# Kernel optimization log

Measured on AMD Instinct MI355X. Metric: run time of the kernel, lower is better.

## Reference

```python
import jax, jax.numpy as jnp
import numpy as np

N = 50000          # nodes
E_RAND = 800000    # random edges
E = E_RAND + N     # + self loops -> 850000
F_IN = 256         # nembed
F_HID = 64         # nhid
H = 8              # nheads
NCLASS = 40
ALPHA = 0.2        # leakyrelu slope


def setup_inputs() -> dict:
    key = jax.random.key(0)
    ks = jax.random.split(key, 8)
    x = jax.random.normal(ks[0], (N, F_IN), dtype=jnp.float32)
    # random edges + self loops (guarantees every row-sum > 0, like adj + I)
    er = jax.random.randint(ks[1], (2, E_RAND), 0, N, dtype=jnp.int32)
    loops = jnp.tile(jnp.arange(N, dtype=jnp.int32)[None, :], (2, 1))
    edge_index = jnp.concatenate([er, loops], axis=1)  # [2, E]
    # per-head attention params (xavier-ish scale)
    W = jax.random.normal(ks[2], (H, F_IN, F_HID), dtype=jnp.float32) * (1.0 / np.sqrt(F_IN))
    a = jax.random.normal(ks[3], (H, 2 * F_HID), dtype=jnp.float32) * 0.1
    Wo = jax.random.normal(ks[4], (H * F_HID, F_HID), dtype=jnp.float32) * (1.0 / np.sqrt(H * F_HID))
    ao = jax.random.normal(ks[5], (2 * F_HID,), dtype=jnp.float32) * 0.1
    mlp_w = jax.random.normal(ks[6], (NCLASS, F_HID), dtype=jnp.float32) * 0.05
    mlp_b = jnp.zeros((NCLASS,), dtype=jnp.float32)
    return {"x": x, "edge_index": edge_index, "W": W, "a": a,
            "Wo": Wo, "ao": ao, "mlp_w": mlp_w, "mlp_b": mlp_b}


def _leaky(v):
    return jnp.where(v > 0, v, ALPHA * v)


def _spgat_layer(x, W, a, src, dst, n):
    """pyGAT SpGraphAttentionLayer (eval mode, dropout = identity).
    out[i] = sum_{e: src=i} exp(-leakyrelu(a.[h_src;h_dst])) * h[dst] / rowsum_i
    """
    h = x @ W                         # [N, D]
    D = W.shape[1]
    s_src = h @ a[:D]                 # [N]
    s_dst = h @ a[D:]                 # [N]
    # per-edge unnormalized attention (note the -exp(leaky) of original sp impl)
    e = jnp.exp(-_leaky(s_src[src] + s_dst[dst]))          # [E]
    rowsum = jax.ops.segment_sum(e, src, num_segments=n)   # [N]
    num = jax.ops.segment_sum(e[:, None] * h[dst], src, num_segments=n)  # [N, D]
    return num / rowsum[:, None]


def reference(x, edge_index, W, a, Wo, ao, mlp_w, mlp_b):
    src, dst = edge_index[0], edge_index[1]
    # multi-head attention, concat=True -> elu inside each head
    heads = [jax.nn.elu(_spgat_layer(x, W[i], a[i], src, dst, N)) for i in range(H)]
    xc = jnp.concatenate(heads, axis=1)                     # [N, H*F_HID]
    # dropout (eval) = identity
    xo = jax.nn.elu(_spgat_layer(xc, Wo, ao, src, dst, N))  # [N, F_HID]
    return xo @ mlp_w.T + mlp_b                             # [N, NCLASS]
```

## Files before the change

kernel.cpp:

```cpp
#include <hip/hip_runtime.h>

#define NN 50000
#define HH 8
#define ALPHA 0.2f
#define NPAD 50048

typedef short short8 __attribute__((ext_vector_type(8)));
typedef float f32x4 __attribute__((ext_vector_type(4)));

__device__ __forceinline__ float elu_f(float x) {
  return x > 0.f ? x : __expf(x) - 1.f;
}

__device__ __forceinline__ unsigned short f2bf(float f) {
  unsigned int u = __float_as_uint(f);
  unsigned int r = (u + 0x7fffu + ((u >> 16) & 1u)) >> 16;
  return (unsigned short)r;
}

__global__ void cvt_all_kernel(const float* __restrict__ x, unsigned short* __restrict__ xb,
                               const float* __restrict__ W, unsigned short* __restrict__ Wtc,
                               const float* __restrict__ Wo, unsigned short* __restrict__ Wot,
                               int* __restrict__ cnt, int N) {
  int tid = blockIdx.x * 256 + threadIdx.x;
  int n4x = NPAD * 64;
  if (tid < n4x) {
    int row = tid >> 6;
    ushort4 o;
    if (row < N) {
      float4 v = ((const float4*)x)[tid];
      o.x = f2bf(v.x); o.y = f2bf(v.y); o.z = f2bf(v.z); o.w = f2bf(v.w);
    } else {
      o.x = o.y = o.z = o.w = 0;
    }
    ((ushort4*)xb)[tid] = o;
    return;
  }
  int t1 = tid - n4x;
  if (t1 < 512 * 256) {
    int c = t1 >> 8, k = t1 & 255;
    int h = c >> 6, cc = c & 63;
    Wtc[t1] = f2bf(W[((size_t)h * 256 + k) * 64 + cc]);
    return;
  }
  int t2 = t1 - 512 * 256;
  if (t2 < 64 * 512) {
    int c = t2 >> 9, k = t2 & 511;
    Wot[t2] = f2bf(Wo[(size_t)k * 64 + c]);
    return;
  }
  int t3 = t2 - 64 * 512;
  if (t3 < N) cnt[t3] = 0;
}

__global__ void hist_kernel(const int* __restrict__ src, int* __restrict__ cnt, int E) {
  int e = blockIdx.x * blockDim.x + threadIdx.x;
  if (e < E) atomicAdd(&cnt[src[e]], 1);
}

__global__ __launch_bounds__(1024) void scan_fused_kernel(const int* __restrict__ cnt,
    int* __restrict__ row_ptr, int* __restrict__ nxt, int n, int E) {
  __shared__ int sh[1024];
  __shared__ int wsum[16];
  __shared__ int base_sh;
  int bid = blockIdx.x;
  int i = (bid << 10) + threadIdx.x;
  int v = (i < n) ? cnt[i] : 0;

  int lim = bid << 10;
  int s = 0;
  for (int q = threadIdx.x; q < lim; q += 1024) s += cnt[q];
#pragma unroll
  for (int off = 1; off < 64; off <<= 1) s += __shfl_xor(s, off, 64);
  if ((threadIdx.x & 63) == 0) wsum[threadIdx.x >> 6] = s;
  sh[threadIdx.x] = v;
  __syncthreads();
  if (threadIdx.x == 0) {
    int t = 0;
#pragma unroll
    for (int j = 0; j < 16; ++j) t += wsum[j];
    base_sh = t;
  }
  for (int off = 1; off < 1024; off <<= 1) {
    int t = (threadIdx.x >= off) ? sh[threadIdx.x - off] : 0;
    __syncthreads();
    sh[threadIdx.x] += t;
    __syncthreads();
  }
  if (i < n) {
    int r = base_sh + sh[threadIdx.x] - v;
    row_ptr[i] = r;
    nxt[i] = r;
  }
  if (i == 0) row_ptr[n] = E;
}

__global__ __launch_bounds__(256) void scatter_gemm1_kernel(
    const int* __restrict__ src, const int* __restrict__ dst,
    int* __restrict__ nxt, int* __restrict__ colv, int E, int eb,
    const unsigned short* __restrict__ A, const unsigned short* __restrict__ Wtc,
    const float* __restrict__ Aatt, unsigned short* __restrict__ Cout,
    float* __restrict__ ss, float* __restrict__ sd, int N) {
  __shared__ unsigned short As[128][40];
  __shared__ unsigned short Bs[128][40];

  if (blockIdx.x < (unsigned)eb) {
    int e = blockIdx.x * 256 + threadIdx.x;
    if (e < E) {
      int p = atomicAdd(&nxt[src[e]], 1);
      colv[p] = dst[e];
    }
    return;
  }

  int tile = blockIdx.x - eb;
  int m0 = (tile >> 2) * 128;
  int c0 = (tile & 3) * 128;
  int w = threadIdx.x >> 6, L = threadIdx.x & 63;
  int quad = L >> 4, l16 = L & 15;
  int wr = w >> 1, wc = w & 1;
  int y = (tile & 3) * 2 + wc;

  f32x4 acc[4][4];
#pragma unroll
  for (int mt = 0; mt < 4; ++mt)
#pragma unroll
    for (int nt = 0; nt < 4; ++nt) acc[mt][nt] = (f32x4)(0.f);

  int sr0 = threadIdx.x >> 2;
  int sk0 = (threadIdx.x & 3) << 3;

  for (int k0 = 0; k0 < 256; k0 += 32) {
    __syncthreads();
    *(uint4*)&As[sr0][sk0]      = *(const uint4*)(A + (size_t)(m0 + sr0) * 256 + k0 + sk0);
    *(uint4*)&As[sr0 + 64][sk0] = *(const uint4*)(A + (size_t)(m0 + sr0 + 64) * 256 + k0 + sk0);
    *(uint4*)&Bs[sr0][sk0]      = *(const uint4*)(Wtc + (size_t)(c0 + sr0) * 256 + k0 + sk0);
    *(uint4*)&Bs[sr0 + 64][sk0] = *(const uint4*)(Wtc + (size_t)(c0 + sr0 + 64) * 256 + k0 + sk0);
    __syncthreads();

    short8 af[4], bf[4];
#pragma unroll
    for (int mt = 0; mt < 4; ++mt)
      af[mt] = *(const short8*)&As[wr * 64 + mt * 16 + l16][quad * 8];
#pragma unroll
    for (int nt = 0; nt < 4; ++nt)
      bf[nt] = *(const short8*)&Bs[wc * 64 + nt * 16 + l16][quad * 8];
#pragma unroll
    for (int mt = 0; mt < 4; ++mt)
#pragma unroll
      for (int nt = 0; nt < 4; ++nt)
        acc[mt][nt] = __builtin_amdgcn_mfma_f32_16x16x32_bf16(af[mt], bf[nt], acc[mt][nt], 0, 0, 0);
  }

  float as[4], ad[4];
#pragma unroll
  for (int nt = 0; nt < 4; ++nt) {
    as[nt] = Aatt[y * 128 + l16 + 16 * nt];
    ad[nt] = Aatt[y * 128 + 64 + l16 + 16 * nt];
  }
#pragma unroll
  for (int mt = 0; mt < 4; ++mt) {
#pragma unroll
    for (int reg = 0; reg < 4; ++reg) {
      int row = m0 + wr * 64 + mt * 16 + quad * 4 + reg;
      float p = 0.f, q = 0.f;
#pragma unroll
      for (int nt = 0; nt < 4; ++nt) {
        p += acc[mt][nt][reg] * as[nt];
        q += acc[mt][nt][reg] * ad[nt];
      }
#pragma unroll
      for (int off = 1; off < 16; off <<= 1) {
        p += __shfl_xor(p, off, 64);
        q += __shfl_xor(q, off, 64);
      }
      if (l16 == 0 && row < N) {
        ss[(size_t)row * 8 + y] = p;
        sd[(size_t)row * 8 + y] = q;
      }
      if (row < N) {
#pragma unroll
        for (int nt = 0; nt < 4; ++nt)
          Cout[(size_t)row * 512 + y * 64 + l16 + 16 * nt] = f2bf(acc[mt][nt][reg]);
      }
    }
  }
}

__global__ __launch_bounds__(256) void mfma_gemm2_kernel(
    const unsigned short* __restrict__ A, const unsigned short* __restrict__ Bt,
    const float* __restrict__ Aatt, unsigned short* __restrict__ Cout,
    float* __restrict__ ss, float* __restrict__ sd, int N) {
  __shared__ unsigned short Bs[64][520];
  unsigned short* stage = &Bs[0][0];
  {
    for (int c = threadIdx.x; c < 4096; c += 256) {
      int n = c >> 6;
      int kq = (c & 63) << 3;
      *(uint4*)&Bs[n][kq] = *(const uint4*)(Bt + (size_t)n * 512 + kq);
    }
  }
  __syncthreads();

  int w = threadIdx.x >> 6, L = threadIdx.x & 63;
  int quad = L >> 4, l16 = L & 15;
  int m0 = blockIdx.x * 64;
  int myrow = m0 + w * 16 + l16;
  const unsigned short* Ar = A + (size_t)myrow * 512 + quad * 8;

  f32x4 acc[4];
#pragma unroll
  for (int nt = 0; nt < 4; ++nt) acc[nt] = (f32x4)(0.f);

  short8 a_cur = *(const short8*)(Ar);
  for (int k0 = 0; k0 < 512; k0 += 32) {
    short8 a_nxt;
    if (k0 + 32 < 512) a_nxt = *(const short8*)(Ar + k0 + 32);
#pragma unroll
    for (int nt = 0; nt < 4; ++nt) {
      short8 b = *(const short8*)&Bs[l16 + 16 * nt][k0 + quad * 8];
      acc[nt] = __builtin_amdgcn_mfma_f32_16x16x32_bf16(a_cur, b, acc[nt], 0, 0, 0);
    }
    a_cur = a_nxt;
  }

  float as[4], ad[4];
#pragma unroll
  for (int nt = 0; nt < 4; ++nt) {
    as[nt] = Aatt[l16 + 16 * nt];
    ad[nt] = Aatt[64 + l16 + 16 * nt];
  }
#pragma unroll
  for (int reg = 0; reg < 4; ++reg) {
    float p = 0.f, q = 0.f;
#pragma unroll
    for (int nt = 0; nt < 4; ++nt) {
      p += acc[nt][reg] * as[nt];
      q += acc[nt][reg] * ad[nt];
    }
#pragma unroll
    for (int off = 1; off < 16; off <<= 1) {
      p += __shfl_xor(p, off, 64);
      q += __shfl_xor(q, off, 64);
    }
    int row = m0 + w * 16 + quad * 4 + reg;
    if (l16 == 0 && row < N) { ss[row] = p; sd[row] = q; }
  }

  __syncthreads();
#pragma unroll
  for (int reg = 0; reg < 4; ++reg) {
    int lrow = w * 16 + quad * 4 + reg;
#pragma unroll
    for (int nt = 0; nt < 4; ++nt)
      stage[lrow * 72 + l16 + 16 * nt] = f2bf(acc[nt][reg]);
  }
  __syncthreads();
#pragma unroll
  for (int i = 0; i < 2; ++i) {
    int idx = threadIdx.x + 256 * i;
    int row = idx >> 3;
    int c8 = (idx & 7) << 3;
    if (m0 + row < N) {
      uint4 v = *(const uint4*)&stage[row * 72 + c8];
      *(uint4*)(Cout + ((size_t)(m0 + row)) * 64 + c8) = v;
    }
  }
}

__global__ __launch_bounds__(256) void agg1_kernel(const unsigned short* __restrict__ table,
    const float* __restrict__ ss, const float* __restrict__ sd,
    const int* __restrict__ row_ptr, const int* __restrict__ col,
    unsigned short* __restrict__ xc, int N) {
  int bid = blockIdx.x;
  int r8 = bid & 7;
  int p = r8 >> 2;
  int nb = ((bid >> 3) << 2) | (r8 & 3);
  int wid = threadIdx.x >> 6, L = threadIdx.x & 63;
  int n = nb * 4 + wid;
  if (n >= N) return;
  int hq = L >> 4;
  int h = p * 4 + hq;
  int el = L & 15;
  float ssn = ss[n * 8 + h];
  int k0 = row_ptr[n], deg = row_ptr[n + 1] - k0;
  float acc[4] = {0.f, 0.f, 0.f, 0.f};
  float rs = 0.f;
  const char* tb = (const char*)table + p * 512;

  for (int c0 = 0; c0 < deg; c0 += 64) {
    int j = c0 + L;
    int d_l = (j < deg) ? col[k0 + j] : 0;
    int m = min(64, deg - c0);
    for (int g = 0; g < m; g += 16) {
      int eoff = g + el;
      int de = __shfl(d_l, eoff, 64);
      float s = ssn + sd[(size_t)de * 8 + h];
      float e = __expf(-fmaxf(s, ALPHA * s));
      if (eoff >= m) e = 0.f;
      rs += e;
      int gm = min(16, m - g);
      uint2 rv[16];
#pragma unroll
      for (int t = 0; t < 16; ++t) {
        if (t < gm) {
          int dg = __builtin_amdgcn_readlane(d_l, g + t);
          rv[t] = *(const uint2*)(tb + (size_t)dg * 1024 + L * 8);
        }
      }
#pragma unroll
      for (int t = 0; t < 16; ++t) {
        if (t < gm) {
          float ew = __shfl(e, (hq << 4) + t, 64);
          acc[0] += ew * __uint_as_float(rv[t].x << 16);
          acc[1] += ew * __uint_as_float(rv[t].x & 0xffff0000u);
          acc[2] += ew * __uint_as_float(rv[t].y << 16);
          acc[3] += ew * __uint_as_float(rv[t].y & 0xffff0000u);
        }
      }
    }
  }
  rs += __shfl_xor(rs, 1, 64);
  rs += __shfl_xor(rs, 2, 64);
  rs += __shfl_xor(rs, 4, 64);
  rs += __shfl_xor(rs, 8, 64);
  float inv = 1.f / rs;
  ushort4 pk;
  pk.x = f2bf(elu_f(acc[0] * inv));
  pk.y = f2bf(elu_f(acc[1] * inv));
  pk.z = f2bf(elu_f(acc[2] * inv));
  pk.w = f2bf(elu_f(acc[3] * inv));
  *(ushort4*)(xc + (size_t)n * 512 + p * 256 + L * 4) = pk;
}

__global__ __launch_bounds__(256) void agg2_final_kernel(const unsigned short* __restrict__ table,
    const float* __restrict__ ss, const float* __restrict__ sd,
    const int* __restrict__ row_ptr, const int* __restrict__ col,
    const float* __restrict__ mlp_w, const float* __restrict__ mlp_b,
    float* __restrict__ out, int N) {
  __shared__ float wsh[40 * 65];
  __shared__ float bsh[40];
  __shared__ float osh[4][68];
  for (int i = threadIdx.x; i < 40 * 64; i += 256) wsh[(i >> 6) * 65 + (i & 63)] = mlp_w[i];
  if (threadIdx.x < 40) bsh[threadIdx.x] = mlp_b[threadIdx.x];
  __syncthreads();

  int wid = threadIdx.x >> 6, L = threadIdx.x & 63;
  int n = blockIdx.x * 4 + wid;
  bool act = (n < N);
  float o = 0.f;
  if (act) {
    float ssn = ss[n];
    int k0 = row_ptr[n], deg = row_ptr[n + 1] - k0;
    float acc = 0.f, rs = 0.f;
    const char* base = (const char*)table;
    for (int c0 = 0; c0 < deg; c0 += 64) {
      int j = c0 + L;
      int d_l = 0;
      float e_l = 0.f;
      if (j < deg) {
        d_l = col[k0 + j];
        float s = ssn + sd[d_l];
        e_l = __expf(-fmaxf(s, ALPHA * s));
      }
      rs += e_l;
      int m = min(64, deg - c0);
      int off_l = d_l << 7;
      for (int g = 0; g < m; g += 16) {
        int gm = min(16, m - g);
        unsigned hv[16];
#pragma unroll
        for (int t = 0; t < 16; ++t) {
          if (t < gm) {
            int so = __builtin_amdgcn_readlane(off_l, g + t);
            hv[t] = *(const unsigned short*)(base + so + L * 2);
          }
        }
#pragma unroll
        for (int t = 0; t < 16; ++t) {
          if (t < gm) {
            float ew = __uint_as_float(
                (unsigned)__builtin_amdgcn_readlane(__float_as_uint(e_l), g + t));
            acc += ew * __uint_as_float(hv[t] << 16);
          }
        }
      }
    }
#pragma unroll
    for (int off = 1; off < 64; off <<= 1) rs += __shfl_xor(rs, off, 64);
    o = elu_f(acc / rs);
  }
  osh[wid][L] = o;
  __syncthreads();
  if (act && L < 40) {
    const float* wr = wsh + L * 65;
    const float* orow = osh[wid];
    float acc = bsh[L];
#pragma unroll
    for (int j = 0; j < 64; ++j) acc += orow[j] * wr[j];
    out[(size_t)n * 40 + L] = acc;
  }
}

extern "C" void kernel_launch(void* const* d_in, const int* in_sizes, int n_in,
                              void* d_out, int out_size, void* d_ws, size_t ws_size,
                              hipStream_t stream) {
  (void)n_in; (void)out_size; (void)ws_size;
  const float* x  = (const float*)d_in[0];
  const int*   ei = (const int*)d_in[1];
  const float* W  = (const float*)d_in[2];
  const float* a  = (const float*)d_in[3];
  const float* Wo = (const float*)d_in[4];
  const float* ao = (const float*)d_in[5];
  const float* mw = (const float*)d_in[6];
  const float* mb = (const float*)d_in[7];
  float* out = (float*)d_out;

  const int N = NN;
  const int E = in_sizes[1] / 2;
  const int* src = ei;
  const int* dst = ei + E;

  char* ws = (char*)d_ws;
  size_t off = 0;
  auto alloc = [&](size_t bytes) {
    char* p = ws + off;
    off = (off + bytes + 255) & ~(size_t)255;
    return p;
  };
  unsigned short* xb  = (unsigned short*)alloc((size_t)NPAD * 256 * 2);
  unsigned short* Wtc = (unsigned short*)alloc((size_t)512 * 256 * 2);
  unsigned short* Wot = (unsigned short*)alloc((size_t)64 * 512 * 2);
  unsigned short* h1b = (unsigned short*)alloc((size_t)N * 512 * 2);
  float* ss1     = (float*)alloc((size_t)N * 8 * 4);
  float* sd1     = (float*)alloc((size_t)N * 8 * 4);
  unsigned short* xc = (unsigned short*)alloc((size_t)NPAD * 512 * 2);
  unsigned short* h2b = (unsigned short*)alloc((size_t)N * 64 * 2);
  float* ss2     = (float*)alloc((size_t)N * 4);
  float* sd2     = (float*)alloc((size_t)N * 4);
  int*   row_ptr = (int*)  alloc((size_t)(N + 1) * 4);
  int*   nxt     = (int*)  alloc((size_t)N * 4);
  int*   cnt     = (int*)  alloc((size_t)N * 4);
  int*   colv    = (int*)  alloc((size_t)E * 4);

  int eb = (E + 255) / 256;
  int nb1024 = (N + 1023) / 1024;
  int cvt_total = NPAD * 64 + 512 * 256 + 64 * 512 + N;
  int gtiles = (NPAD / 128) * 4;

  hipLaunchKernelGGL(cvt_all_kernel, dim3((cvt_total + 255) / 256), dim3(256), 0, stream,
                     x, xb, W, Wtc, Wo, Wot, cnt, N);

  hipLaunchKernelGGL(hist_kernel, dim3(eb), dim3(256), 0, stream, src, cnt, E);
  hipLaunchKernelGGL(scan_fused_kernel, dim3(nb1024), dim3(1024), 0, stream,
                     cnt, row_ptr, nxt, N, E);

  hipLaunchKernelGGL(scatter_gemm1_kernel, dim3(eb + gtiles), dim3(256), 0, stream,
                     src, dst, nxt, colv, E, eb,
                     xb, Wtc, a, h1b, ss1, sd1, N);

  hipLaunchKernelGGL(agg1_kernel, dim3(2 * ((N + 3) / 4)), dim3(256), 0, stream,
                     h1b, ss1, sd1, row_ptr, colv, xc, N);

  hipLaunchKernelGGL(mfma_gemm2_kernel, dim3(NPAD / 64), dim3(256), 0, stream,
                     xc, Wot, ao, h2b, ss2, sd2, N);
  hipLaunchKernelGGL(agg2_final_kernel, dim3((N + 3) / 4), dim3(256), 0, stream,
                     h2b, ss2, sd2, row_ptr, colv, mw, mb, out, N);
}
```

Baseline: 442.1 us.

## Fuse all stages into one persistent cooperative mega-kernel with grid syncs

Replaces the seven separate launches (convert, histogram, scan, scatter+GEMM1, aggregation 1, GEMM2, aggregation 2 + MLP) with a single cooperative persistent kernel that strides over work and uses grid.sync between phases. The scan is reworked to 256 threads handling 4 elements each, and GEMM2 now uses 128-row tiles staged through shared memory instead of holding the full weight matrix in LDS. The aim is to remove launch gaps and tail effects between kernels. The cost is that every phase is bound by the occupancy-limited persistent grid (launch bounds of 4 blocks per CU, capped at 8), and grid-wide barriers plus fences are added.

```diff
diff --git a/kernel.cpp b/kernel.cpp
--- a/kernel.cpp
+++ b/kernel.cpp
@@ -1,4 +1,7 @@
 #include <hip/hip_runtime.h>
+#include <hip/hip_cooperative_groups.h>
+
+namespace cg = cooperative_groups;
 
 #define NN 50000
 #define HH 8
@@ -18,387 +21,405 @@
   return (unsigned short)r;
 }
 
-__global__ void cvt_all_kernel(const float* __restrict__ x, unsigned short* __restrict__ xb,
-                               const float* __restrict__ W, unsigned short* __restrict__ Wtc,
-                               const float* __restrict__ Wo, unsigned short* __restrict__ Wot,
-                               int* __restrict__ cnt, int N) {
-  int tid = blockIdx.x * 256 + threadIdx.x;
-  int n4x = NPAD * 64;
-  if (tid < n4x) {
-    int row = tid >> 6;
-    ushort4 o;
-    if (row < N) {
-      float4 v = ((const float4*)x)[tid];
-      o.x = f2bf(v.x); o.y = f2bf(v.y); o.z = f2bf(v.z); o.w = f2bf(v.w);
-    } else {
-      o.x = o.y = o.z = o.w = 0;
-    }
-    ((ushort4*)xb)[tid] = o;
-    return;
-  }
-  int t1 = tid - n4x;
-  if (t1 < 512 * 256) {
-    int c = t1 >> 8, k = t1 & 255;
-    int h = c >> 6, cc = c & 63;
-    Wtc[t1] = f2bf(W[((size_t)h * 256 + k) * 64 + cc]);
-    return;
-  }
-  int t2 = t1 - 512 * 256;
-  if (t2 < 64 * 512) {
-    int c = t2 >> 9, k = t2 & 511;
-    Wot[t2] = f2bf(Wo[(size_t)k * 64 + c]);
-    return;
-  }
-  int t3 = t2 - 64 * 512;
-  if (t3 < N) cnt[t3] = 0;
-}
-
-__global__ void hist_kernel(const int* __restrict__ src, int* __restrict__ cnt, int E) {
-  int e = blockIdx.x * blockDim.x + threadIdx.x;
-  if (e < E) atomicAdd(&cnt[src[e]], 1);
-}
-
-__global__ __launch_bounds__(1024) void scan_fused_kernel(const int* __restrict__ cnt,
-    int* __restrict__ row_ptr, int* __restrict__ nxt, int n, int E) {
-  __shared__ int sh[1024];
-  __shared__ int wsum[16];
-  __shared__ int base_sh;
-  int bid = blockIdx.x;
-  int i = (bid << 10) + threadIdx.x;
-  int v = (i < n) ? cnt[i] : 0;
-
-  int lim = bid << 10;
-  int s = 0;
-  for (int q = threadIdx.x; q < lim; q += 1024) s += cnt[q];
-#pragma unroll
-  for (int off = 1; off < 64; off <<= 1) s += __shfl_xor(s, off, 64);
-  if ((threadIdx.x & 63) == 0) wsum[threadIdx.x >> 6] = s;
-  sh[threadIdx.x] = v;
-  __syncthreads();
-  if (threadIdx.x == 0) {
-    int t = 0;
-#pragma unroll
-    for (int j = 0; j < 16; ++j) t += wsum[j];
-    base_sh = t;
-  }
-  for (int off = 1; off < 1024; off <<= 1) {
-    int t = (threadIdx.x >= off) ? sh[threadIdx.x - off] : 0;
+__global__ __launch_bounds__(256, 4) void mega_kernel(
+    const float* __restrict__ x, const int* __restrict__ esrc, const int* __restrict__ edst,
+    const float* __restrict__ W, const float* __restrict__ Aatt,
+    const float* __restrict__ Wo, const float* __restrict__ ao,
+    const float* __restrict__ mw, const float* __restrict__ mb, float* __restrict__ out,
+    unsigned short* __restrict__ xb, unsigned short* __restrict__ Wtc,
+    unsigned short* __restrict__ Wot, unsigned short* __restrict__ h1b,
+    float* __restrict__ ss1, float* __restrict__ sd1,
+    unsigned short* __restrict__ xc, unsigned short* __restrict__ h2b,
+    float* __restrict__ ss2, float* __restrict__ sd2,
+    int* __restrict__ row_ptr, int* __restrict__ nxt, int* __restrict__ cnt,
+    int* __restrict__ colv, int E) {
+  __shared__ __align__(16) char smem[20480];
+  cg::grid_group grid = cg::this_grid();
+  const int tid = threadIdx.x;
+  const int gsz = gridDim.x;
+
+  {
+    const int n4x = NPAD * 64;
+    const int total = n4x + 512 * 256 + 64 * 512 + NN;
+    for (int t = blockIdx.x * 256 + tid; t < total; t += gsz * 256) {
+      if (t < n4x) {
+        int row = t >> 6;
+        ushort4 o;
+        if (row < NN) {
+          float4 v = ((const float4*)x)[t];
+          o.x = f2bf(v.x); o.y = f2bf(v.y); o.z = f2bf(v.z); o.w = f2bf(v.w);
+        } else {
+          o.x = o.y = o.z = o.w = 0;
+        }
+        ((ushort4*)xb)[t] = o;
+      } else {
+        int t1 = t - n4x;
+        if (t1 < 512 * 256) {
+          int c = t1 >> 8, k = t1 & 255;
+          int h = c >> 6, cc = c & 63;
+          Wtc[t1] = f2bf(W[((size_t)h * 256 + k) * 64 + cc]);
+        } else {
+          int t2 = t1 - 512 * 256;
+          if (t2 < 64 * 512) {
+            int c = t2 >> 9, k = t2 & 511;
+            Wot[t2] = f2bf(Wo[(size_t)k * 64 + c]);
+          } else {
+            int t3 = t2 - 64 * 512;
+            if (t3 < NN) cnt[t3] = 0;
+          }
+        }
+      }
+    }
+  }
+  __threadfence();
+  grid.sync();
+
+  for (int e = blockIdx.x * 256 + tid; e < E; e += gsz * 256)
+    atomicAdd(&cnt[esrc[e]], 1);
+  __threadfence();
+  grid.sync();
+
+  {
+    int* sh = (int*)smem;
+    const int nch = (NN + 1023) >> 10;
+    for (int chunk = blockIdx.x; chunk < nch; chunk += gsz) {
+      int lim = chunk << 10;
+      int s = 0;
+      for (int q = tid; q < lim; q += 256) s += cnt[q];
+#pragma unroll
+      for (int off = 1; off < 64; off <<= 1) s += __shfl_xor(s, off, 64);
+      int i0 = lim + (tid << 2);
+      int v0 = (i0     < NN) ? cnt[i0]     : 0;
+      int v1 = (i0 + 1 < NN) ? cnt[i0 + 1] : 0;
+      int v2 = (i0 + 2 < NN) ? cnt[i0 + 2] : 0;
+      int v3 = (i0 + 3 < NN) ? cnt[i0 + 3] : 0;
+      int tsum = v0 + v1 + v2 + v3;
+      __syncthreads();
+      if ((tid & 63) == 0) sh[256 + (tid >> 6)] = s;
+      sh[tid] = tsum;
+      __syncthreads();
+      for (int off = 1; off < 256; off <<= 1) {
+        int tv = (tid >= off) ? sh[tid - off] : 0;
+        __syncthreads();
+        sh[tid] += tv;
+        __syncthreads();
+      }
+      int base = sh[256] + sh[257] + sh[258] + sh[259];
+      int r = base + sh[tid] - tsum;
+      if (i0     < NN) { row_ptr[i0]     = r; nxt[i0]     = r; } r += v0;
+      if (i0 + 1 < NN) { row_ptr[i0 + 1] = r; nxt[i0 + 1] = r; } r += v1;
+      if (i0 + 2 < NN) { row_ptr[i0 + 2] = r; nxt[i0 + 2] = r; } r += v2;
+      if (i0 + 3 < NN) { row_ptr[i0 + 3] = r; nxt[i0 + 3] = r; }
+      __syncthreads();
+    }
+    if (blockIdx.x == 0 && tid == 0) row_ptr[NN] = E;
+  }
+  __threadfence();
+  grid.sync();
+
+  {
+    const int eb = (E + 255) >> 8;
+    const int gtiles = (NPAD / 128) * 4;
+    typedef unsigned short (*Arr40)[40];
+    Arr40 As = (Arr40)smem;
+    Arr40 Bs = (Arr40)(smem + 10240);
+    const int w = tid >> 6, L = tid & 63;
+    const int quad = L >> 4, l16 = L & 15;
+    const int wr = w >> 1, wc = w & 1;
+    const int sr0 = tid >> 2;
+    const int sk0 = (tid & 3) << 3;
+
+    for (int vb = blockIdx.x; vb < eb + gtiles; vb += gsz) {
+      if (vb < eb) {
+        int e = vb * 256 + tid;
+        if (e < E) {
+          int p = atomicAdd(&nxt[esrc[e]], 1);
+          colv[p] = edst[e];
+        }
+        continue;
+      }
+      int tile = vb - eb;
+      int m0 = (tile >> 2) * 128;
+      int c0 = (tile & 3) * 128;
+      int y = (tile & 3) * 2 + wc;
+
+      f32x4 acc[4][4];
+#pragma unroll
+      for (int mt = 0; mt < 4; ++mt)
+#pragma unroll
+        for (int nt = 0; nt < 4; ++nt) acc[mt][nt] = (f32x4)(0.f);
+
+      for (int k0 = 0; k0 < 256; k0 += 32) {
+        __syncthreads();
+        *(uint4*)&As[sr0][sk0]      = *(const uint4*)(xb + (size_t)(m0 + sr0) * 256 + k0 + sk0);
+        *(uint4*)&As[sr0 + 64][sk0] = *(const uint4*)(xb + (size_t)(m0 + sr0 + 64) * 256 + k0 + sk0);
+        *(uint4*)&Bs[sr0][sk0]      = *(const uint4*)(Wtc + (size_t)(c0 + sr0) * 256 + k0 + sk0);
+        *(uint4*)&Bs[sr0 + 64][sk0] = *(const uint4*)(Wtc + (size_t)(c0 + sr0 + 64) * 256 + k0 + sk0);
+        __syncthreads();
+
+        short8 af[4], bf[4];
+#pragma unroll
+        for (int mt = 0; mt < 4; ++mt)
+          af[mt] = *(const short8*)&As[wr * 64 + mt * 16 + l16][quad * 8];
+#pragma unroll
+        for (int nt = 0; nt < 4; ++nt)
+          bf[nt] = *(const short8*)&Bs[wc * 64 + nt * 16 + l16][quad * 8];
+#pragma unroll
+        for (int mt = 0; mt < 4; ++mt)
+#pragma unroll
+          for (int nt = 0; nt < 4; ++nt)
+            acc[mt][nt] = __builtin_amdgcn_mfma_f32_16x16x32_bf16(af[mt], bf[nt], acc[mt][nt], 0, 0, 0);
+      }
+
+      float as[4], ad[4];
+#pragma unroll
+      for (int nt = 0; nt < 4; ++nt) {
+        as[nt] = Aatt[y * 128 + l16 + 16 * nt];
+        ad[nt] = Aatt[y * 128 + 64 + l16 + 16 * nt];
+      }
+#pragma unroll
+      for (int mt = 0; mt < 4; ++mt) {
+#pragma unroll
+        for (int reg = 0; reg < 4; ++reg) {
+          int row = m0 + wr * 64 + mt * 16 + quad * 4 + reg;
+          float p = 0.f, q = 0.f;
+#pragma unroll
+          for (int nt = 0; nt < 4; ++nt) {
+            p += acc[mt][nt][reg] * as[nt];
+            q += acc[mt][nt][reg] * ad[nt];
+          }
+#pragma unroll
+          for (int off = 1; off < 16; off <<= 1) {
+            p += __shfl_xor(p, off, 64);
+            q += __shfl_xor(q, off, 64);
+          }
+          if (l16 == 0 && row < NN) {
+            ss1[(size_t)row * 8 + y] = p;
+            sd1[(size_t)row * 8 + y] = q;
+          }
+          if (row < NN) {
+#pragma unroll
+            for (int nt = 0; nt < 4; ++nt)
+              h1b[(size_t)row * 512 + y * 64 + l16 + 16 * nt] = f2bf(acc[mt][nt][reg]);
+          }
+        }
+      }
+    }
+  }
+  __threadfence();
+  grid.sync();
+
+  {
+    const int nbb = (NN + 3) / 4;
+    const int wid = tid >> 6, L = tid & 63;
+    const int hq = L >> 4;
+    const int el = L & 15;
+    for (int vb = blockIdx.x; vb < 2 * nbb; vb += gsz) {
+      int r8 = vb & 7;
+      int p = r8 >> 2;
+      int nb = ((vb >> 3) << 2) | (r8 & 3);
+      int n = nb * 4 + wid;
+      if (n >= NN) continue;
+      int h = p * 4 + hq;
+      float ssn = ss1[n * 8 + h];
+      int k0 = row_ptr[n], deg = row_ptr[n + 1] - k0;
+      float acc[4] = {0.f, 0.f, 0.f, 0.f};
+      float rs = 0.f;
+      const char* tb = (const char*)h1b + p * 512;
+
+      for (int c0 = 0; c0 < deg; c0 += 64) {
+        int j = c0 + L;
+        int d_l = (j < deg) ? colv[k0 + j] : 0;
+        int m = min(64, deg - c0);
+        for (int g = 0; g < m; g += 16) {
+          int eoff = g + el;
+          int de = __shfl(d_l, eoff, 64);
+          float s = ssn + sd1[(size_t)de * 8 + h];
+          float e = __expf(-fmaxf(s, ALPHA * s));
+          if (eoff >= m) e = 0.f;
+          rs += e;
+          int gm = min(16, m - g);
+          uint2 rv[16];
+#pragma unroll
+          for (int t = 0; t < 16; ++t) {
+            if (t < gm) {
+              int dg = __builtin_amdgcn_readlane(d_l, g + t);
+              rv[t] = *(const uint2*)(tb + (size_t)dg * 1024 + L * 8);
+            }
+          }
+#pragma unroll
+          for (int t = 0; t < 16; ++t) {
+            if (t < gm) {
+              float ew = __shfl(e, (hq << 4) + t, 64);
+              acc[0] += ew * __uint_as_float(rv[t].x << 16);
+              acc[1] += ew * __uint_as_float(rv[t].x & 0xffff0000u);
+              acc[2] += ew * __uint_as_float(rv[t].y << 16);
+              acc[3] += ew * __uint_as_float(rv[t].y & 0xffff0000u);
+            }
+          }
+        }
+      }
+      rs += __shfl_xor(rs, 1, 64);
+      rs += __shfl_xor(rs, 2, 64);
+      rs += __shfl_xor(rs, 4, 64);
+      rs += __shfl_xor(rs, 8, 64);
+      float inv = 1.f / rs;
+      ushort4 pk;
+      pk.x = f2bf(elu_f(acc[0] * inv));
+      pk.y = f2bf(elu_f(acc[1] * inv));
+      pk.z = f2bf(elu_f(acc[2] * inv));
+      pk.w = f2bf(elu_f(acc[3] * inv));
+      *(ushort4*)(xc + (size_t)n * 512 + p * 256 + L * 4) = pk;
+    }
+  }
+  __threadfence();
+  grid.sync();
+
+  {
+    typedef unsigned short (*Arr40)[40];
+    Arr40 As = (Arr40)smem;
+    Arr40 Bs2 = (Arr40)(smem + 10240);
+    const int ntiles = NPAD / 128;
+    const int w = tid >> 6, L = tid & 63;
+    const int quad = L >> 4, l16 = L & 15;
+
+    float as[4], ad[4];
+#pragma unroll
+    for (int nt = 0; nt < 4; ++nt) {
+      as[nt] = ao[l16 + 16 * nt];
+      ad[nt] = ao[64 + l16 + 16 * nt];
+    }
+
+    for (int tile = blockIdx.x; tile < ntiles; tile += gsz) {
+      int m0 = tile * 128;
+      f32x4 acc[2][4];
+#pragma unroll
+      for (int mt = 0; mt < 2; ++mt)
+#pragma unroll
+        for (int nt = 0; nt < 4; ++nt) acc[mt][nt] = (f32x4)(0.f);
+
+      for (int k0 = 0; k0 < 512; k0 += 32) {
+        __syncthreads();
+        {
+          int idx = tid;
+          int r0 = idx >> 2, kq = (idx & 3) << 3;
+          *(uint4*)&As[r0][kq] = *(const uint4*)(xc + (size_t)(m0 + r0) * 512 + k0 + kq);
+          idx = tid + 256; r0 = idx >> 2; kq = (idx & 3) << 3;
+          *(uint4*)&As[r0][kq] = *(const uint4*)(xc + (size_t)(m0 + r0) * 512 + k0 + kq);
+          int n2 = tid >> 2, kq2 = (tid & 3) << 3;
+          *(uint4*)&Bs2[n2][kq2] = *(const uint4*)(Wot + (size_t)n2 * 512 + k0 + kq2);
+        }
+        __syncthreads();
+
+        short8 af[2], bf[4];
+        af[0] = *(const short8*)&As[w * 32 + l16][quad * 8];
+        af[1] = *(const short8*)&As[w * 32 + 16 + l16][quad * 8];
+#pragma unroll
+        for (int nt = 0; nt < 4; ++nt)
+          bf[nt] = *(const short8*)&Bs2[nt * 16 + l16][quad * 8];
+#pragma unroll
+        for (int mt = 0; mt < 2; ++mt)
+#pragma unroll
+          for (int nt = 0; nt < 4; ++nt)
+            acc[mt][nt] = __builtin_amdgcn_mfma_f32_16x16x32_bf16(af[mt], bf[nt], acc[mt][nt], 0, 0, 0);
+      }
+
+#pragma unroll
+      for (int mt = 0; mt < 2; ++mt) {
+#pragma unroll
+        for (int reg = 0; reg < 4; ++reg) {
+          int row = m0 + w * 32 + mt * 16 + quad * 4 + reg;
+          float p = 0.f, q = 0.f;
+#pragma unroll
+          for (int nt = 0; nt < 4; ++nt) {
+            p += acc[mt][nt][reg] * as[nt];
+            q += acc[mt][nt][reg] * ad[nt];
+          }
+#pragma unroll
+          for (int off = 1; off < 16; off <<= 1) {
+            p += __shfl_xor(p, off, 64);
+            q += __shfl_xor(q, off, 64);
+          }
+          if (l16 == 0 && row < NN) { ss2[row] = p; sd2[row] = q; }
+          if (row < NN) {
+#pragma unroll
+            for (int nt = 0; nt < 4; ++nt)
+              h2b[(size_t)row * 64 + l16 + 16 * nt] = f2bf(acc[mt][nt][reg]);
+          }
+        }
+      }
+    }
+  }
+  __threadfence();
+  grid.sync();
+
+  {
+    float* wsh = (float*)smem;
+    float* bsh = wsh + 40 * 65;
+    float (*osh)[68] = (float(*)[68])(bsh + 40);
+    for (int i = tid; i < 40 * 64; i += 256) wsh[(i >> 6) * 65 + (i & 63)] = mw[i];
+    if (tid < 40) bsh[tid] = mb[tid];
     __syncthreads();
-    sh[threadIdx.x] += t;
-    __syncthreads();
-  }
-  if (i < n) {
-    int r = base_sh + sh[threadIdx.x] - v;
-    row_ptr[i] = r;
-    nxt[i] = r;
-  }
-  if (i == 0) row_ptr[n] = E;
-}
-
-__global__ __launch_bounds__(256) void scatter_gemm1_kernel(
-    const int* __restrict__ src, const int* __restrict__ dst,
-    int* __restrict__ nxt, int* __restrict__ colv, int E, int eb,
-    const unsigned short* __restrict__ A, const unsigned short* __restrict__ Wtc,
-    const float* __restrict__ Aatt, unsigned short* __restrict__ Cout,
-    float* __restrict__ ss, float* __restrict__ sd, int N) {
-  __shared__ unsigned short As[128][40];
-  __shared__ unsigned short Bs[128][40];
-
-  if (blockIdx.x < (unsigned)eb) {
-    int e = blockIdx.x * 256 + threadIdx.x;
-    if (e < E) {
-      int p = atomicAdd(&nxt[src[e]], 1);
-      colv[p] = dst[e];
-    }
-    return;
-  }
-
-  int tile = blockIdx.x - eb;
-  int m0 = (tile >> 2) * 128;
-  int c0 = (tile & 3) * 128;
-  int w = threadIdx.x >> 6, L = threadIdx.x & 63;
-  int quad = L >> 4, l16 = L & 15;
-  int wr = w >> 1, wc = w & 1;
-  int y = (tile & 3) * 2 + wc;
-
-  f32x4 acc[4][4];
-#pragma unroll
-  for (int mt = 0; mt < 4; ++mt)
-#pragma unroll
-    for (int nt = 0; nt < 4; ++nt) acc[mt][nt] = (f32x4)(0.f);
-
-  int sr0 = threadIdx.x >> 2;
-  int sk0 = (threadIdx.x & 3) << 3;
-
-  for (int k0 = 0; k0 < 256; k0 += 32) {
-    __syncthreads();
-    *(uint4*)&As[sr0][sk0]      = *(const uint4*)(A + (size_t)(m0 + sr0) * 256 + k0 + sk0);
-    *(uint4*)&As[sr0 + 64][sk0] = *(const uint4*)(A + (size_t)(m0 + sr0 + 64) * 256 + k0 + sk0);
-    *(uint4*)&Bs[sr0][sk0]      = *(const uint4*)(Wtc + (size_t)(c0 + sr0) * 256 + k0 + sk0);
-    *(uint4*)&Bs[sr0 + 64][sk0] = *(const uint4*)(Wtc + (size_t)(c0 + sr0 + 64) * 256 + k0 + sk0);
-    __syncthreads();
-
-    short8 af[4], bf[4];
-#pragma unroll
-    for (int mt = 0; mt < 4; ++mt)
-      af[mt] = *(const short8*)&As[wr * 64 + mt * 16 + l16][quad * 8];
-#pragma unroll
-    for (int nt = 0; nt < 4; ++nt)
-      bf[nt] = *(const short8*)&Bs[wc * 64 + nt * 16 + l16][quad * 8];
-#pragma unroll
-    for (int mt = 0; mt < 4; ++mt)
-#pragma unroll
-      for (int nt = 0; nt < 4; ++nt)
-        acc[mt][nt] = __builtin_amdgcn_mfma_f32_16x16x32_bf16(af[mt], bf[nt], acc[mt][nt], 0, 0, 0);
-  }
-
-  float as[4], ad[4];
-#pragma unroll
-  for (int nt = 0; nt < 4; ++nt) {
-    as[nt] = Aatt[y * 128 + l16 + 16 * nt];
-    ad[nt] = Aatt[y * 128 + 64 + l16 + 16 * nt];
-  }
-#pragma unroll
-  for (int mt = 0; mt < 4; ++mt) {
-#pragma unroll
-    for (int reg = 0; reg < 4; ++reg) {
-      int row = m0 + wr * 64 + mt * 16 + quad * 4 + reg;
-      float p = 0.f, q = 0.f;
-#pragma unroll
-      for (int nt = 0; nt < 4; ++nt) {
-        p += acc[mt][nt][reg] * as[nt];
-        q += acc[mt][nt][reg] * ad[nt];
-      }
-#pragma unroll
-      for (int off = 1; off < 16; off <<= 1) {
-        p += __shfl_xor(p, off, 64);
-        q += __shfl_xor(q, off, 64);
-      }
-      if (l16 == 0 && row < N) {
-        ss[(size_t)row * 8 + y] = p;
-        sd[(size_t)row * 8 + y] = q;
-      }
-      if (row < N) {
-#pragma unroll
-        for (int nt = 0; nt < 4; ++nt)
-          Cout[(size_t)row * 512 + y * 64 + l16 + 16 * nt] = f2bf(acc[mt][nt][reg]);
-      }
-    }
-  }
-}
-
-__global__ __launch_bounds__(256) void mfma_gemm2_kernel(
-    const unsigned short* __restrict__ A, const unsigned short* __restrict__ Bt,
-    const float* __restrict__ Aatt, unsigned short* __restrict__ Cout,
-    float* __restrict__ ss, float* __restrict__ sd, int N) {
-  __shared__ unsigned short Bs[64][520];
-  unsigned short* stage = &Bs[0][0];
-  {
-    for (int c = threadIdx.x; c < 4096; c += 256) {
-      int n = c >> 6;
-      int kq = (c & 63) << 3;
-      *(uint4*)&Bs[n][kq] = *(const uint4*)(Bt + (size_t)n * 512 + kq);
-    }
-  }
-  __syncthreads();
-
-  int w = threadIdx.x >> 6, L = threadIdx.x & 63;
-  int quad = L >> 4, l16 = L & 15;
-  int m0 = blockIdx.x * 64;
-  int myrow = m0 + w * 16 + l16;
-  const unsigned short* Ar = A + (size_t)myrow * 512 + quad * 8;
-
-  f32x4 acc[4];
-#pragma unroll
-  for (int nt = 0; nt < 4; ++nt) acc[nt] = (f32x4)(0.f);
-
-  short8 a_cur = *(const short8*)(Ar);
-  for (int k0 = 0; k0 < 512; k0 += 32) {
-    short8 a_nxt;
-    if (k0 + 32 < 512) a_nxt = *(const short8*)(Ar + k0 + 32);
-#pragma unroll
-    for (int nt = 0; nt < 4; ++nt) {
-      short8 b = *(const short8*)&Bs[l16 + 16 * nt][k0 + quad * 8];
-      acc[nt] = __builtin_amdgcn_mfma_f32_16x16x32_bf16(a_cur, b, acc[nt], 0, 0, 0);
-    }
-    a_cur = a_nxt;
-  }
-
-  float as[4], ad[4];
-#pragma unroll
-  for (int nt = 0; nt < 4; ++nt) {
-    as[nt] = Aatt[l16 + 16 * nt];
-    ad[nt] = Aatt[64 + l16 + 16 * nt];
-  }
-#pragma unroll
-  for (int reg = 0; reg < 4; ++reg) {
-    float p = 0.f, q = 0.f;
-#pragma unroll
-    for (int nt = 0; nt < 4; ++nt) {
-      p += acc[nt][reg] * as[nt];
-      q += acc[nt][reg] * ad[nt];
-    }
-#pragma unroll
-    for (int off = 1; off < 16; off <<= 1) {
-      p += __shfl_xor(p, off, 64);
-      q += __shfl_xor(q, off, 64);
-    }
-    int row = m0 + w * 16 + quad * 4 + reg;
-    if (l16 == 0 && row < N) { ss[row] = p; sd[row] = q; }
-  }
-
-  __syncthreads();
-#pragma unroll
-  for (int reg = 0; reg < 4; ++reg) {
-    int lrow = w * 16 + quad * 4 + reg;
-#pragma unroll
-    for (int nt = 0; nt < 4; ++nt)
-      stage[lrow * 72 + l16 + 16 * nt] = f2bf(acc[nt][reg]);
-  }
-  __syncthreads();
-#pragma unroll
-  for (int i = 0; i < 2; ++i) {
-    int idx = threadIdx.x + 256 * i;
-    int row = idx >> 3;
-    int c8 = (idx & 7) << 3;
-    if (m0 + row < N) {
-      uint4 v = *(const uint4*)&stage[row * 72 + c8];
-      *(uint4*)(Cout + ((size_t)(m0 + row)) * 64 + c8) = v;
-    }
-  }
-}
-
-__global__ __launch_bounds__(256) void agg1_kernel(const unsigned short* __restrict__ table,
-    const float* __restrict__ ss, const float* __restrict__ sd,
-    const int* __restrict__ row_ptr, const int* __restrict__ col,
-    unsigned short* __restrict__ xc, int N) {
-  int bid = blockIdx.x;
-  int r8 = bid & 7;
-  int p = r8 >> 2;
-  int nb = ((bid >> 3) << 2) | (r8 & 3);
-  int wid = threadIdx.x >> 6, L = threadIdx.x & 63;
-  int n = nb * 4 + wid;
-  if (n >= N) return;
-  int hq = L >> 4;
-  int h = p * 4 + hq;
-  int el = L & 15;
-  float ssn = ss[n * 8 + h];
-  int k0 = row_ptr[n], deg = row_ptr[n + 1] - k0;
-  float acc[4] = {0.f, 0.f, 0.f, 0.f};
-  float rs = 0.f;
-  const char* tb = (const char*)table + p * 512;
-
-  for (int c0 = 0; c0 < deg; c0 += 64) {
-    int j = c0 + L;
-    int d_l = (j < deg) ? col[k0 + j] : 0;
-    int m = min(64, deg - c0);
-    for (int g = 0; g < m; g += 16) {
-      int eoff = g + el;
-      int de = __shfl(d_l, eoff, 64);
-      float s = ssn + sd[(size_t)de * 8 + h];
-      float e = __expf(-fmaxf(s, ALPHA * s));
-      if (eoff >= m) e = 0.f;
-      rs += e;
-      int gm = min(16, m - g);
-      uint2 rv[16];
-#pragma unroll
-      for (int t = 0; t < 16; ++t) {
-        if (t < gm) {
-          int dg = __builtin_amdgcn_readlane(d_l, g + t);
-          rv[t] = *(const uint2*)(tb + (size_t)dg * 1024 + L * 8);
-        }
-      }
-#pragma unroll
-      for (int t = 0; t < 16; ++t) {
-        if (t < gm) {
-          float ew = __shfl(e, (hq << 4) + t, 64);
-          acc[0] += ew * __uint_as_float(rv[t].x << 16);
-          acc[1] += ew * __uint_as_float(rv[t].x & 0xffff0000u);
-          acc[2] += ew * __uint_as_float(rv[t].y << 16);
-          acc[3] += ew * __uint_as_float(rv[t].y & 0xffff0000u);
-        }
-      }
-    }
-  }
-  rs += __shfl_xor(rs, 1, 64);
-  rs += __shfl_xor(rs, 2, 64);
-  rs += __shfl_xor(rs, 4, 64);
-  rs += __shfl_xor(rs, 8, 64);
-  float inv = 1.f / rs;
-  ushort4 pk;
-  pk.x = f2bf(elu_f(acc[0] * inv));
-  pk.y = f2bf(elu_f(acc[1] * inv));
-  pk.z = f2bf(elu_f(acc[2] * inv));
-  pk.w = f2bf(elu_f(acc[3] * inv));
-  *(ushort4*)(xc + (size_t)n * 512 + p * 256 + L * 4) = pk;
-}
-
-__global__ __launch_bounds__(256) void agg2_final_kernel(const unsigned short* __restrict__ table,
-    const float* __restrict__ ss, const float* __restrict__ sd,
-    const int* __restrict__ row_ptr, const int* __restrict__ col,
-    const float* __restrict__ mlp_w, const float* __restrict__ mlp_b,
-    float* __restrict__ out, int N) {
-  __shared__ float wsh[40 * 65];
-  __shared__ float bsh[40];
-  __shared__ float osh[4][68];
-  for (int i = threadIdx.x; i < 40 * 64; i += 256) wsh[(i >> 6) * 65 + (i & 63)] = mlp_w[i];
-  if (threadIdx.x < 40) bsh[threadIdx.x] = mlp_b[threadIdx.x];
-  __syncthreads();
-
-  int wid = threadIdx.x >> 6, L = threadIdx.x & 63;
-  int n = blockIdx.x * 4 + wid;
-  bool act = (n < N);
-  float o = 0.f;
-  if (act) {
-    float ssn = ss[n];
-    int k0 = row_ptr[n], deg = row_ptr[n + 1] - k0;
-    float acc = 0.f, rs = 0.f;
-    const char* base = (const char*)table;
-    for (int c0 = 0; c0 < deg; c0 += 64) {
-      int j = c0 + L;
-      int d_l = 0;
-      float e_l = 0.f;
-      if (j < deg) {
-        d_l = col[k0 + j];
-        float s = ssn + sd[d_l];
-        e_l = __expf(-fmaxf(s, ALPHA * s));
-      }
-      rs += e_l;
-      int m = min(64, deg - c0);
-      int off_l = d_l << 7;
-      for (int g = 0; g < m; g += 16) {
-        int gm = min(16, m - g);
-        unsigned hv[16];
-#pragma unroll
-        for (int t = 0; t < 16; ++t) {
-          if (t < gm) {
-            int so = __builtin_amdgcn_readlane(off_l, g + t);
-            hv[t] = *(const unsigned short*)(base + so + L * 2);
-          }
-        }
-#pragma unroll
-        for (int t = 0; t < 16; ++t) {
-          if (t < gm) {
-            float ew = __uint_as_float(
-                (unsigned)__builtin_amdgcn_readlane(__float_as_uint(e_l), g + t));
-            acc += ew * __uint_as_float(hv[t] << 16);
-          }
-        }
-      }
-    }
-#pragma unroll
-    for (int off = 1; off < 64; off <<= 1) rs += __shfl_xor(rs, off, 64);
-    o = elu_f(acc / rs);
-  }
-  osh[wid][L] = o;
-  __syncthreads();
-  if (act && L < 40) {
-    const float* wr = wsh + L * 65;
-    const float* orow = osh[wid];
-    float acc = bsh[L];
-#pragma unroll
-    for (int j = 0; j < 64; ++j) acc += orow[j] * wr[j];
-    out[(size_t)n * 40 + L] = acc;
+
+    const int nbb = (NN + 3) / 4;
+    const int wid = tid >> 6, L = tid & 63;
+    for (int vb = blockIdx.x; vb < nbb; vb += gsz) {
+      int n = vb * 4 + wid;
+      bool act = (n < NN);
+      float o = 0.f;
+      if (act) {
+        float ssn = ss2[n];
+        int k0 = row_ptr[n], deg = row_ptr[n + 1] - k0;
+        float acc = 0.f, rs = 0.f;
+        const char* base = (const char*)h2b;
+        for (int c0 = 0; c0 < deg; c0 += 64) {
+          int j = c0 + L;
+          int d_l = 0;
+          float e_l = 0.f;
+          if (j < deg) {
+            d_l = colv[k0 + j];
+            float s = ssn + sd2[d_l];
+            e_l = __expf(-fmaxf(s, ALPHA * s));
+          }
+          rs += e_l;
+          int m = min(64, deg - c0);
+          int off_l = d_l << 7;
+          for (int g = 0; g < m; g += 16) {
+            int gm = min(16, m - g);
+            unsigned hv[16];
+#pragma unroll
+            for (int t = 0; t < 16; ++t) {
+              if (t < gm) {
+                int so = __builtin_amdgcn_readlane(off_l, g + t);
+                hv[t] = *(const unsigned short*)(base + so + L * 2);
+              }
+            }
+#pragma unroll
+            for (int t = 0; t < 16; ++t) {
+              if (t < gm) {
+                float ew = __uint_as_float(
+                    (unsigned)__builtin_amdgcn_readlane(__float_as_uint(e_l), g + t));
+                acc += ew * __uint_as_float(hv[t] << 16);
+              }
+            }
+          }
+        }
+#pragma unroll
+        for (int off = 1; off < 64; off <<= 1) rs += __shfl_xor(rs, off, 64);
+        o = elu_f(acc / rs);
+      }
+      osh[wid][L] = o;
+      __syncthreads();
+      if (act && L < 40) {
+        const float* wr = wsh + L * 65;
+        const float* orow = osh[wid];
+        float acc = bsh[L];
+#pragma unroll
+        for (int j = 0; j < 64; ++j) acc += orow[j] * wr[j];
+        out[(size_t)n * 40 + L] = acc;
+      }
+      __syncthreads();
+    }
   }
 }
 
@@ -417,7 +438,7 @@
   float* out = (float*)d_out;
 
   const int N = NN;
-  const int E = in_sizes[1] / 2;
+  int E = in_sizes[1] / 2;
   const int* src = ei;
   const int* dst = ei + E;
 
@@ -443,27 +464,18 @@
   int*   cnt     = (int*)  alloc((size_t)N * 4);
   int*   colv    = (int*)  alloc((size_t)E * 4);
 
-  int eb = (E + 255) / 256;
-  int nb1024 = (N + 1023) / 1024;
-  int cvt_total = NPAD * 64 + 512 * 256 + 64 * 512 + N;
-  int gtiles = (NPAD / 128) * 4;
-
-  hipLaunchKernelGGL(cvt_all_kernel, dim3((cvt_total + 255) / 256), dim3(256), 0, stream,
-                     x, xb, W, Wtc, Wo, Wot, cnt, N);
-
-  hipLaunchKernelGGL(hist_kernel, dim3(eb), dim3(256), 0, stream, src, cnt, E);
-  hipLaunchKernelGGL(scan_fused_kernel, dim3(nb1024), dim3(1024), 0, stream,
-                     cnt, row_ptr, nxt, N, E);
-
-  hipLaunchKernelGGL(scatter_gemm1_kernel, dim3(eb + gtiles), dim3(256), 0, stream,
-                     src, dst, nxt, colv, E, eb,
-                     xb, Wtc, a, h1b, ss1, sd1, N);
-
-  hipLaunchKernelGGL(agg1_kernel, dim3(2 * ((N + 3) / 4)), dim3(256), 0, stream,
-                     h1b, ss1, sd1, row_ptr, colv, xc, N);
-
-  hipLaunchKernelGGL(mfma_gemm2_kernel, dim3(NPAD / 64), dim3(256), 0, stream,
-                     xc, Wot, ao, h2b, ss2, sd2, N);
-  hipLaunchKernelGGL(agg2_final_kernel, dim3((N + 3) / 4), dim3(256), 0, stream,
-                     h2b, ss2, sd2, row_ptr, colv, mw, mb, out, N);
+  int maxb = 0;
+  hipOccupancyMaxActiveBlocksPerMultiprocessor(&maxb, mega_kernel, 256, 0);
+  if (maxb < 1) maxb = 1;
+  if (maxb > 8) maxb = 8;
+  int gridsz = maxb * 256;
+
+  void* args[] = {
+    (void*)&x, (void*)&src, (void*)&dst, (void*)&W, (void*)&a, (void*)&Wo,
+    (void*)&ao, (void*)&mw, (void*)&mb, (void*)&out,
+    (void*)&xb, (void*)&Wtc, (void*)&Wot, (void*)&h1b, (void*)&ss1, (void*)&sd1,
+    (void*)&xc, (void*)&h2b, (void*)&ss2, (void*)&sd2,
+    (void*)&row_ptr, (void*)&nxt, (void*)&cnt, (void*)&colv, (void*)&E
+  };
+  hipLaunchCooperativeKernel(mega_kernel, dim3(gridsz), dim3(256), args, 0, stream);
 }
```

Measured after the change: 1.191 ms. 2.69x slower.
